# Performance work log

Hardware: AMD Instinct MI355X
Metric: run time of the kernel (lower is better)

## Reference

```python
import jax, jax.numpy as jnp
import numpy as np

DIM = 256; D_STATE = 16; D_CONV = 4; EXPAND = 2; NS = 64
D_INNER = EXPAND * DIM; DT_RANK = (DIM + 15) // 16
B_SZ = 2; H = 64; W = 64


def setup_inputs() -> dict:
    key = jax.random.key(0)
    ks = jax.random.split(key, 32)
    g = lambda i, shape, s=0.02: jax.random.normal(ks[i], shape, dtype=jnp.float32) * s
    inp = {}
    inp["x"] = jax.random.normal(ks[0], (B_SZ, DIM, H, W), dtype=jnp.float32)
    inp["ln_w"] = jnp.ones((DIM,), jnp.float32)
    inp["ln_b"] = jnp.zeros((DIM,), jnp.float32)
    inp["in_proj_w"] = g(1, (2 * D_INNER, DIM))
    for suf, base in (("", 2), ("_b", 10), ("_s", 18)):
        inp["conv_w" + suf] = g(base, (D_INNER, D_CONV), 0.1)
        inp["conv_b" + suf] = g(base + 1, (D_INNER,), 0.1)
        inp["x_proj_w" + suf] = g(base + 2, (DT_RANK + 2 * D_STATE, D_INNER))
        inp["dt_proj_w" + suf] = g(base + 3, (D_INNER, DT_RANK), 0.1)
        inp["dt_proj_b" + suf] = g(base + 4, (D_INNER,), 0.5)
        inp["D" + suf] = jnp.ones((D_INNER,), jnp.float32)
    A_log = jnp.tile(jnp.log(jnp.arange(1, D_STATE + 1, dtype=jnp.float32)), (D_INNER, 1))
    inp["A_log"] = A_log
    inp["A_log_b"] = A_log
    inp["A_log_s"] = A_log
    inp["out_proj_w"] = g(26, (DIM, D_INNER))
    return inp


def _silu(x):
    return x * jax.nn.sigmoid(x)


def _causal_conv(x, w, b):
    # x: (B, L, D); w: (D, K) depthwise causal conv along L
    K = w.shape[1]; L = x.shape[1]
    xp = jnp.pad(x, ((0, 0), (K - 1, 0), (0, 0)))
    y = b
    for k in range(K):
        y = y + xp[:, k:k + L, :] * w[:, k]
    return y


def _ssm_dir(x, z, conv_w, conv_b, x_proj_w, dt_proj_w, dt_proj_b, A_log, Dp):
    # one directional Mamba inner fn (no out_proj); x, z: (B, L, d_inner)
    Bsz, L, Din = x.shape
    xc = _silu(_causal_conv(x, conv_w, conv_b))
    x_dbl = xc @ x_proj_w.T  # (B, L, dt_rank + 2*d_state)
    dt_r = x_dbl[..., :DT_RANK]
    Bm = x_dbl[..., DT_RANK:DT_RANK + D_STATE]
    Cm = x_dbl[..., DT_RANK + D_STATE:]
    dt = jax.nn.softplus(dt_r @ dt_proj_w.T + dt_proj_b)  # (B, L, d_inner)
    A = -jnp.exp(A_log)  # (d_inner, d_state)

    def step(h, inp):
        dt_t, x_t, B_t, C_t = inp
        dA = jnp.exp(dt_t[..., None] * A)  # (B, d_inner, d_state)
        h = dA * h + (dt_t * x_t)[..., None] * B_t[:, None, :]
        return h, jnp.einsum('bds,bs->bd', h, C_t)

    h0 = jnp.zeros((Bsz, Din, D_STATE), x.dtype)
    _, ys = jax.lax.scan(step, h0, (dt.transpose(1, 0, 2), xc.transpose(1, 0, 2),
                                    Bm.transpose(1, 0, 2), Cm.transpose(1, 0, 2)))
    y = ys.transpose(1, 0, 2) + xc * Dp
    return y * _silu(z)


def reference(x, ln_w, ln_b, in_proj_w,
              conv_w, conv_b, x_proj_w, dt_proj_w, dt_proj_b, D,
              conv_w_b, conv_b_b, x_proj_w_b, dt_proj_w_b, dt_proj_b_b, D_b,
              conv_w_s, conv_b_s, x_proj_w_s, dt_proj_w_s, dt_proj_b_s, D_s,
              A_log, A_log_b, A_log_s, out_proj_w):
    Bsz, C, Hh, Ww = x.shape
    L = Hh * Ww
    xf = x.reshape(Bsz, C, L).transpose(0, 2, 1)  # (B, L, C)
    mu = xf.mean(-1, keepdims=True)
    var = ((xf - mu) ** 2).mean(-1, keepdims=True)
    xn = (xf - mu) / jnp.sqrt(var + 1e-5) * ln_w + ln_b
    xz = xn @ in_proj_w.T  # (B, L, 2*d_inner), shared across directions
    xin, z = xz[..., :D_INNER], xz[..., D_INNER:]
    # forward scan
    y_f = _ssm_dir(xin, z, conv_w, conv_b, x_proj_w, dt_proj_w, dt_proj_b, A_log, D)
    # backward scan (flip sequence, scan, flip back)
    y_b = _ssm_dir(xin[:, ::-1], z[:, ::-1], conv_w_b, conv_b_b, x_proj_w_b,
                   dt_proj_w_b, dt_proj_b_b, A_log_b, D_b)[:, ::-1]
    # slice-interleaved scan: 'b (s i) d -> b (i s) d' with s = NS slices
    def il(t):
        return t.reshape(Bsz, NS, L // NS, D_INNER).transpose(0, 2, 1, 3).reshape(Bsz, L, D_INNER)
    def dil(t):
        return t.reshape(Bsz, L // NS, NS, D_INNER).transpose(0, 2, 1, 3).reshape(Bsz, L, D_INNER)
    y_s = dil(_ssm_dir(il(xin), il(z), conv_w_s, conv_b_s, x_proj_w_s,
                       dt_proj_w_s, dt_proj_b_s, A_log_s, D_s))
    out = (y_f + y_b + y_s) @ out_proj_w.T  # (B, L, C)
    return x + out.transpose(0, 2, 1).reshape(Bsz, C, Hh, Ww)
```

## Files before the change

### kernel.cpp

```cpp
#include <hip/hip_runtime.h>
#include <hip/hip_bf16.h>
#include <cstdint>

#define B_SZ 2
#define DIM 256
#define L_SEQ 4096
#define D_INNER 512
#define DT_RANK 16
#define D_STATE 16
#define NCHUNK 128
#define CHUNK 32

static constexpr size_t SZ_BIG_SH = (size_t)B_SZ * L_SEQ * D_INNER;
static constexpr size_t F_DIR  = (size_t)B_SZ * NCHUNK * D_STATE * D_INNER;
static constexpr size_t SD_DIR = (size_t)B_SZ * NCHUNK * D_INNER;

typedef __attribute__((ext_vector_type(8))) short short8v;
typedef __attribute__((ext_vector_type(4))) short short4v;
typedef __attribute__((ext_vector_type(4))) float f32x4;

__device__ __forceinline__ float silu_f(float v) {
    return v / (1.0f + __expf(-v));
}
__device__ __forceinline__ float softplus_fast(float v) {
    return (v > 15.0f) ? v : __logf(1.0f + __expf(v));
}
__device__ __forceinline__ short f2bf(float f) {
    uint32_t u = __float_as_uint(f);
    u += 0x7fffu + ((u >> 16) & 1u);
    return (short)(u >> 16);
}
__device__ __forceinline__ float bf2f(short s) {
    return __uint_as_float(((uint32_t)(uint16_t)s) << 16);
}
__device__ __forceinline__ int dir_map(int p, int dm) {
    if (dm == 0) return p;
    if (dm == 1) return (L_SEQ - 1) - p;
    return ((p & 63) << 6) | (p >> 6);
}
__device__ __forceinline__ void pow_dA(float r1, float* dA) {
    const float r2 = r1 * r1, r4 = r2 * r2, r8 = r4 * r4;
    dA[0] = r1;         dA[1] = r2;         dA[2] = r2 * r1;    dA[3] = r4;
    dA[4] = r4 * r1;    dA[5] = r4 * r2;    dA[6] = r4 * dA[2]; dA[7] = r8;
    dA[8] = r8 * r1;    dA[9] = r8 * r2;    dA[10] = r8 * dA[2]; dA[11] = r8 * r4;
    dA[12] = r8 * dA[4]; dA[13] = r8 * dA[5]; dA[14] = r8 * dA[6]; dA[15] = r8 * r8;
}

__global__ __launch_bounds__(256) void k_cvt(
    const float* __restrict__ Wi, const float* __restrict__ Wo,
    const float* __restrict__ xp0, const float* __restrict__ xp1, const float* __restrict__ xp2,
    const float* __restrict__ dw0, const float* __restrict__ dw1, const float* __restrict__ dw2,
    short* __restrict__ Wib, short* __restrict__ Wob,
    short* __restrict__ xpwb, short* __restrict__ dtwb)
{
    const int idx = blockIdx.x * 256 + threadIdx.x;
    const float* src; short* dst; int off;
    if (idx < 65536)        { src = Wi; dst = Wib; off = idx; }
    else if (idx < 98304)   { src = Wo; dst = Wob; off = idx - 65536; }
    else if (idx < 116736)  {
        int k = idx - 98304; const int d = k / 6144; k -= d * 6144;
        src = d == 0 ? xp0 : (d == 1 ? xp1 : xp2);
        dst = xpwb + (size_t)d * 24576; off = k;
    } else {
        int k = idx - 116736; const int d = k / 2048; k -= d * 2048;
        src = d == 0 ? dw0 : (d == 1 ? dw1 : dw2);
        dst = dtwb + (size_t)d * 8192; off = k;
    }
    const float4 v = *(const float4*)(src + (size_t)off * 4);
    short4v p = {f2bf(v.x), f2bf(v.y), f2bf(v.z), f2bf(v.w)};
    *(short4v*)(dst + (size_t)off * 4) = p;
}

__global__ __launch_bounds__(256) void k_ln_t(
    const float* __restrict__ x, const float* __restrict__ lnw,
    const float* __restrict__ lnb, short* __restrict__ xnb)
{
    __shared__ float xt[64][257];
    __shared__ float red[2][4][64];
    __shared__ float muS[64], rsS[64];
    __shared__ float lnwS[DIM], lnbS[DIM];

    const int b  = blockIdx.x >> 6;
    const int l0 = (blockIdx.x & 63) << 6;
    const int t  = threadIdx.x;
    lnwS[t] = lnw[t]; lnbS[t] = lnb[t];

    const float* xb = x + (size_t)b * DIM * L_SEQ + l0;
#pragma unroll
    for (int it = 0; it < 16; ++it) {
        const int idx = it * 256 + t;
        const int c = idx >> 4, pos = (idx & 15) << 2;
        const float4 v = *(const float4*)(xb + (size_t)c * L_SEQ + pos);
        xt[pos + 0][c] = v.x; xt[pos + 1][c] = v.y;
        xt[pos + 2][c] = v.z; xt[pos + 3][c] = v.w;
    }
    __syncthreads();
    {
        const int l = t & 63, cq = t >> 6;
        float sum = 0.f, sq = 0.f;
        for (int c = cq * 64; c < cq * 64 + 64; ++c) {
            const float v = xt[l][c];
            sum += v; sq += v * v;
        }
        red[0][cq][l] = sum; red[1][cq][l] = sq;
    }
    __syncthreads();
    if (t < 64) {
        const float s  = red[0][0][t] + red[0][1][t] + red[0][2][t] + red[0][3][t];
        const float q2 = red[1][0][t] + red[1][1][t] + red[1][2][t] + red[1][3][t];
        const float mu  = s * (1.0f / DIM);
        const float var = q2 * (1.0f / DIM) - mu * mu;
        muS[t] = mu; rsS[t] = rsqrtf(var + 1e-5f);
    }
    __syncthreads();
#pragma unroll
    for (int it = 0; it < 32; ++it) {
        const int idx = it * 256 + t;
        const int l = idx >> 7, cp = (idx & 127) << 1;
        const float mu = muS[l], rs = rsS[l];
        short2 p;
        p.x = f2bf((xt[l][cp + 0] - mu) * rs * lnwS[cp + 0] + lnbS[cp + 0]);
        p.y = f2bf((xt[l][cp + 1] - mu) * rs * lnwS[cp + 1] + lnbS[cp + 1]);
        *(short2*)(xnb + (size_t)((b * L_SEQ) + l0 + l) * DIM + cp) = p;
    }
}

__global__ __launch_bounds__(256) void k_inproj_mfma(
    const short* __restrict__ xnb, const short* __restrict__ Wib,
    short* __restrict__ xinb, short* __restrict__ szb)
{
    const int mblk = blockIdx.x >> 2;
    const int q    = blockIdx.x & 3;
    const int t = threadIdx.x;
    const int w = t >> 6, l = t & 63;
    const int m0 = mblk * 64 + w * 16;
    const int n0 = q * 256;
    const int lrow = l & 15, lk = l >> 4;

    short8v a[8];
    {
        const short* ap = xnb + (size_t)(m0 + lrow) * DIM + lk * 8;
#pragma unroll
        for (int kk = 0; kk < 8; ++kk)
            a[kk] = *(const short8v*)(ap + kk * 32);
    }

#pragma unroll 4
    for (int nf = 0; nf < 16; ++nf) {
        const int n = n0 + nf * 16 + lrow;
        const short* bp = Wib + (size_t)n * DIM + lk * 8;
        f32x4 acc = {0.f, 0.f, 0.f, 0.f};
#pragma unroll
        for (int kk = 0; kk < 8; ++kk)
            acc = __builtin_amdgcn_mfma_f32_16x16x32_bf16(
                a[kk], *(const short8v*)(bp + kk * 32), acc, 0, 0, 0);
        const int col = n;
        const int r0  = m0 + lk * 4;
        if (n0 < D_INNER) {
#pragma unroll
            for (int j = 0; j < 4; ++j)
                xinb[(size_t)(r0 + j) * D_INNER + col] = f2bf(acc[j]);
        } else {
#pragma unroll
            for (int j = 0; j < 4; ++j)
                szb[(size_t)(r0 + j) * D_INNER + (col - D_INNER)] = f2bf(silu_f(acc[j]));
        }
    }
}

__global__ __launch_bounds__(256) void k_conv3(
    const short* __restrict__ xinb,
    const float* __restrict__ cw0, const float* __restrict__ cw1, const float* __restrict__ cw2,
    const float* __restrict__ cb0, const float* __restrict__ cb1, const float* __restrict__ cb2,
    short* __restrict__ xcbb, int dir_base, size_t xcb_str)
{
    const int rel = blockIdx.x >> 9;
    const int rem = blockIdx.x & 511;
    const int dir = dir_base + rel;
    const int b   = rem >> 8;
    const int p0  = (rem & 255) << 4;
    const int t   = threadIdx.x;

    const float* cw = dir == 0 ? cw0 : (dir == 1 ? cw1 : cw2);
    const float* cb = dir == 0 ? cb0 : (dir == 1 ? cb1 : cb2);
    short* xcb = xcbb + (size_t)rel * xcb_str;

    __shared__ short s[19][D_INNER];
    for (int i = 0; i < 19; ++i) {
        const int pk = p0 - 3 + i;
        short2 v = {0, 0};
        if (pk >= 0) {
            const int lo = dir_map(pk, dir);
            v = *(const short2*)(xinb + ((size_t)b * L_SEQ + lo) * D_INNER + t * 2);
        }
        *(short2*)&s[i][t * 2] = v;
    }
    __syncthreads();

#pragma unroll
    for (int half = 0; half < 2; ++half) {
        const int d = half * 256 + t;
        const float4 wv = *(const float4*)(cw + d * 4);
        const float bb = cb[d];
        float x0 = bf2f(s[0][d]), x1 = bf2f(s[1][d]), x2 = bf2f(s[2][d]);
#pragma unroll
        for (int i = 0; i < 16; ++i) {
            const float x3 = bf2f(s[i + 3][d]);
            const float a = bb + wv.x * x0 + wv.y * x1 + wv.z * x2 + wv.w * x3;
            xcb[((size_t)b * L_SEQ + p0 + i) * D_INNER + d] = f2bf(silu_f(a));
            x0 = x1; x1 = x2; x2 = x3;
        }
    }
}

__global__ __launch_bounds__(256) void k_proj3_mfma(
    const short* __restrict__ xcbb, const short* __restrict__ xpwb,
    const short* __restrict__ dtwb,
    const float* __restrict__ dtb0, const float* __restrict__ dtb1, const float* __restrict__ dtb2,
    short* __restrict__ dtYb, float* __restrict__ bcbuf,
    int dir_base, size_t xcb_str, size_t bc_str)
{
    const int rel = blockIdx.x >> 9;
    const int rem = blockIdx.x & 511;
    const int dir = dir_base + rel;
    const int m0  = rem * 16;
    const int t = threadIdx.x;
    const int w = t >> 6, l = t & 63;
    const int lrow = l & 15, lk = l >> 4;

    const short* xcb = xcbb + (size_t)rel * xcb_str;
    const short* xpw = xpwb + (size_t)dir * (48 * 512);
    const short* dtw = dtwb + (size_t)dir * (512 * 16);
    const float* dtb = dir == 0 ? dtb0 : (dir == 1 ? dtb1 : dtb2);
    short* dt = dtYb + (size_t)dir * SZ_BIG_SH;
    float* bc = bcbuf + (size_t)rel * bc_str;

    __shared__ float red[4][3][16][17];
    __shared__ short xdblb[16][16];
    __shared__ float dtbS[512];

    dtbS[t] = dtb[t]; dtbS[t + 256] = dtb[t + 256];

    short8v a[4];
    {
        const short* ap = xcb + (size_t)(m0 + lrow) * D_INNER + w * 128 + lk * 8;
#pragma unroll
        for (int kk = 0; kk < 4; ++kk)
            a[kk] = *(const short8v*)(ap + kk * 32);
    }

#pragma unroll
    for (int nf = 0; nf < 3; ++nf) {
        f32x4 acc = {0.f, 0.f, 0.f, 0.f};
        const short* bp = xpw + (size_t)(nf * 16 + lrow) * D_INNER + w * 128 + lk * 8;
#pragma unroll
        for (int kk = 0; kk < 4; ++kk)
            acc = __builtin_amdgcn_mfma_f32_16x16x32_bf16(
                a[kk], *(const short8v*)(bp + kk * 32), acc, 0, 0, 0);
#pragma unroll
        for (int j = 0; j < 4; ++j)
            red[w][nf][lk * 4 + j][lrow] = acc[j];
    }
    __syncthreads();

#pragma unroll
    for (int i = 0; i < 3; ++i) {
        const int nf = i;
        const int row = (t >> 4) & 15, col = t & 15;
        const float v = red[0][nf][row][col] + red[1][nf][row][col]
                      + red[2][nf][row][col] + red[3][nf][row][col];
        if (nf == 0) xdblb[row][col] = f2bf(v);
        else         bc[(size_t)(m0 + row) * 32 + (nf - 1) * 16 + col] = v;
    }
    __syncthreads();

    short8v adt = {0, 0, 0, 0, 0, 0, 0, 0};
    if (lk < 2) adt = *(const short8v*)&xdblb[lrow][lk * 8];

#pragma unroll
    for (int nbw = 0; nbw < 8; ++nbw) {
        const int nb = w * 8 + nbw;
        short8v bdt = {0, 0, 0, 0, 0, 0, 0, 0};
        if (lk < 2) bdt = *(const short8v*)(dtw + (size_t)(nb * 16 + lrow) * 16 + lk * 8);
        f32x4 acc = {0.f, 0.f, 0.f, 0.f};
        acc = __builtin_amdgcn_mfma_f32_16x16x32_bf16(adt, bdt, acc, 0, 0, 0);
        const int d = nb * 16 + lrow;
        const float bias = dtbS[d];
#pragma unroll
        for (int j = 0; j < 4; ++j)
            dt[(size_t)(m0 + lk * 4 + j) * D_INNER + d] = f2bf(softplus_fast(acc[j] + bias));
    }
}

__device__ __forceinline__ bool fast_vote(const float* Al_d, int t, int* flagS) {
    bool ok = true;
    const float a0 = __expf(Al_d[0]);
#pragma unroll
    for (int s = 1; s < 16; ++s) {
        const float v = __expf(Al_d[s]);
        const float e = (float)(s + 1) * a0;
        ok = ok && (fabsf(v - e) <= 1e-3f * e);
    }
    if (t == 0) *flagS = 1;
    __syncthreads();
    if (!ok) *flagS = 0;
    __syncthreads();
    return *flagS != 0;
}

template<bool FAST>
__device__ __forceinline__ void scan1_body(
    const short* dtp, const short* xcp, const float* bcp,
    short (*dts)[256], short (*xcs)[256], float (*bcs)[16],
    const float* Al_d, int t, float* F_o, float* SD_o)
{
    float As20, As2[16];
    if (FAST) {
        As20 = -__expf(Al_d[0]) * 1.44269504f;
    } else {
#pragma unroll
        for (int s = 0; s < 16; ++s) As2[s] = -__expf(Al_d[s]) * 1.44269504f;
        As20 = As2[0];
    }
    float h[16];
#pragma unroll
    for (int s = 0; s < 16; ++s) h[s] = 0.f;
    float sumdt = 0.f;

    for (int tile = 0; tile < CHUNK / 16; ++tile) {
        const int p0 = tile * 16;
#pragma unroll
        for (int rep = 0; rep < 2; ++rep) {
            const int idx = rep * 256 + t;
            const int jr = idx >> 5, c8 = (idx & 31) << 3;
            *(short8v*)&dts[jr][c8] = *(const short8v*)(dtp + (size_t)(p0 + jr) * D_INNER + c8);
            *(short8v*)&xcs[jr][c8] = *(const short8v*)(xcp + (size_t)(p0 + jr) * D_INNER + c8);
        }
        if (t < 64) {
            const int jr = t >> 2, c4 = (t & 3) << 2;
            *(float4*)&bcs[jr][c4] = *(const float4*)(bcp + (size_t)(p0 + jr) * 32 + c4);
        }
        __syncthreads();

#pragma unroll
        for (int j = 0; j < 16; ++j) {
            const float dtv = bf2f(dts[j][t]);
            const float xv  = bf2f(xcs[j][t]);
            sumdt += dtv;
            const float dtx = dtv * xv;
            float Bv[16];
#pragma unroll
            for (int s4 = 0; s4 < 4; ++s4) {
                const float4 bb = *(const float4*)&bcs[j][s4 * 4];
                Bv[s4 * 4 + 0] = bb.x; Bv[s4 * 4 + 1] = bb.y;
                Bv[s4 * 4 + 2] = bb.z; Bv[s4 * 4 + 3] = bb.w;
            }
            if (FAST) {
                float dA[16];
                pow_dA(exp2f(dtv * As20), dA);
#pragma unroll
                for (int s = 0; s < 16; ++s)
                    h[s] = fmaf(dA[s], h[s], dtx * Bv[s]);
            } else {
#pragma unroll
                for (int s = 0; s < 16; ++s)
                    h[s] = fmaf(exp2f(dtv * As2[s]), h[s], dtx * Bv[s]);
            }
        }
        __syncthreads();
    }
#pragma unroll
    for (int s = 0; s < 16; ++s)
        F_o[(size_t)s * D_INNER] = h[s];
    *SD_o = sumdt;
}

template<bool FAST>
__device__ __forceinline__ void scan2_body(
    short* dtp, const short* xcp, const float* bcp,
    short (*dts)[256], short (*xcs)[256], float (*bcs)[32],
    const float* Al_d, int t, float Dv, const float* Hin_o)
{
    float As20, As2[16];
    if (FAST) {
        As20 = -__expf(Al_d[0]) * 1.44269504f;
    } else {
#pragma unroll
        for (int s = 0; s < 16; ++s) As2[s] = -__expf(Al_d[s]) * 1.44269504f;
        As20 = As2[0];
    }
    float h[16];
#pragma unroll
    for (int s = 0; s < 16; ++s)
        h[s] = Hin_o[(size_t)s * D_INNER];

    for (int tile = 0; tile < CHUNK / 16; ++tile) {
        const int p0 = tile * 16;
#pragma unroll
        for (int rep = 0; rep < 2; ++rep) {
            const int idx = rep * 256 + t;
            const int jr = idx >> 5, c8 = (idx & 31) << 3;
            *(short8v*)&dts[jr][c8] = *(const short8v*)(dtp + (size_t)(p0 + jr) * D_INNER + c8);
            *(short8v*)&xcs[jr][c8] = *(const short8v*)(xcp + (size_t)(p0 + jr) * D_INNER + c8);
        }
        if (t < 128) {
            const int jr = t >> 3, c4 = (t & 7) << 2;
            *(float4*)&bcs[jr][c4] = *(const float4*)(bcp + (size_t)(p0 + jr) * 32 + c4);
        }
        __syncthreads();

#pragma unroll
        for (int j = 0; j < 16; ++j) {
            const float dtv = bf2f(dts[j][t]);
            const float xv  = bf2f(xcs[j][t]);
            const float dtx = dtv * xv;
            float Bv[16], Cv[16];
#pragma unroll
            for (int s4 = 0; s4 < 4; ++s4) {
                const float4 bb = *(const float4*)&bcs[j][s4 * 4];
                const float4 cc = *(const float4*)&bcs[j][16 + s4 * 4];
                Bv[s4 * 4 + 0] = bb.x; Bv[s4 * 4 + 1] = bb.y;
                Bv[s4 * 4 + 2] = bb.z; Bv[s4 * 4 + 3] = bb.w;
                Cv[s4 * 4 + 0] = cc.x; Cv[s4 * 4 + 1] = cc.y;
                Cv[s4 * 4 + 2] = cc.z; Cv[s4 * 4 + 3] = cc.w;
            }
            float y = xv * Dv;
            if (FAST) {
                float dA[16];
                pow_dA(exp2f(dtv * As20), dA);
#pragma unroll
                for (int s = 0; s < 16; ++s) {
                    h[s] = fmaf(dA[s], h[s], dtx * Bv[s]);
                    y = fmaf(h[s], Cv[s], y);
                }
            } else {
#pragma unroll
                for (int s = 0; s < 16; ++s) {
                    h[s] = fmaf(exp2f(dtv * As2[s]), h[s], dtx * Bv[s]);
                    y = fmaf(h[s], Cv[s], y);
                }
            }
            dtp[(size_t)(p0 + j) * D_INNER + t] = f2bf(y);
        }
        __syncthreads();
    }
}

__global__ __launch_bounds__(256, 4) void k_scan1(
    const short* __restrict__ dtYb, const short* __restrict__ xcbb,
    const float* __restrict__ bcb,
    const float* __restrict__ Al0, const float* __restrict__ Al1, const float* __restrict__ Al2,
    float* __restrict__ Fg, float* __restrict__ SDg,
    int dir_base, size_t xcb_str, size_t bc_str)
{
    const int rel = blockIdx.x >> 9;
    const int rem = blockIdx.x & 511;
    const int dir = dir_base + rel;
    const int b     = rem >> 8;
    const int chunk = (rem >> 1) & 127;
    const int half  = rem & 1;
    const int t = threadIdx.x;
    const int d = half * 256 + t;

    const short* dtg = dtYb + (size_t)dir * SZ_BIG_SH;
    const short* xcg = xcbb + (size_t)rel * xcb_str;
    const float* bcg = bcb + (size_t)rel * bc_str;
    const float* Al = dir == 0 ? Al0 : (dir == 1 ? Al1 : Al2);
    float* F  = Fg  + (size_t)rel * F_DIR;
    float* SD = SDg + (size_t)rel * SD_DIR;

    __shared__ short dts[16][256];
    __shared__ short xcs[16][256];
    __shared__ float bcs[16][16];
    __shared__ int flagS;

    const size_t rowbase = (size_t)b * L_SEQ + chunk * CHUNK;
    const short* dtp = dtg + rowbase * D_INNER + half * 256;
    const short* xcp = xcg + rowbase * D_INNER + half * 256;
    const float* bcp = bcg + rowbase * 32;
    const float* Al_d = Al + d * D_STATE;
    const size_t fo  = ((size_t)b * NCHUNK + chunk) * (D_STATE * D_INNER) + d;
    const size_t sdo = ((size_t)b * NCHUNK + chunk) * D_INNER + d;

    const bool fast = fast_vote(Al_d, t, &flagS);
    if (fast) scan1_body<true >(dtp, xcp, bcp, dts, xcs, bcs, Al_d, t, F + fo, SD + sdo);
    else      scan1_body<false>(dtp, xcp, bcp, dts, xcs, bcs, Al_d, t, F + fo, SD + sdo);
}

__global__ __launch_bounds__(256) void k_comb(
    float* __restrict__ Fg, const float* __restrict__ SDg,
    const float* __restrict__ Al0, const float* __restrict__ Al1, const float* __restrict__ Al2,
    int dir_base)
{
    const int rel = blockIdx.x >> 6;
    const int dir = dir_base + rel;
    const int gid = (blockIdx.x & 63) * 256 + threadIdx.x;
    const int b   = gid >> 13;
    const int rem = gid & 8191;
    const int s   = rem >> 9;
    const int d   = rem & 511;

    const float* Al = dir == 0 ? Al0 : (dir == 1 ? Al1 : Al2);
    const float As2 = -__expf(Al[d * D_STATE + s]) * 1.44269504f;

    float* F        = Fg  + (size_t)rel * F_DIR;
    const float* SD = SDg + (size_t)rel * SD_DIR;

    float h = 0.f;
    for (int c = 0; c < NCHUNK; ++c) {
        const size_t base = (size_t)(b * NCHUNK + c);
        const size_t i  = (base << 13) + rem;
        const float sd  = SD[(base << 9) + d];
        const float P   = exp2f(As2 * sd);
        const float fv  = F[i];
        F[i] = h;
        h = fmaf(P, h, fv);
    }
}

__global__ __launch_bounds__(256, 4) void k_scan2(
    short* dtYb,
    const short* __restrict__ xcbb, const float* __restrict__ bcb,
    const float* __restrict__ Al0, const float* __restrict__ Al1, const float* __restrict__ Al2,
    const float* __restrict__ Dp0, const float* __restrict__ Dp1, const float* __restrict__ Dp2,
    const float* __restrict__ Hing,
    int dir_base, size_t xcb_str, size_t bc_str)
{
    const int rel = blockIdx.x >> 9;
    const int rem = blockIdx.x & 511;
    const int dir = dir_base + rel;
    const int b     = rem >> 8;
    const int chunk = (rem >> 1) & 127;
    const int half  = rem & 1;
    const int t = threadIdx.x;
    const int d = half * 256 + t;

    short* dtg      = dtYb + (size_t)dir * SZ_BIG_SH;
    const short* xcg = xcbb + (size_t)rel * xcb_str;
    const float* bcg = bcb + (size_t)rel * bc_str;
    const float* Al  = dir == 0 ? Al0 : (dir == 1 ? Al1 : Al2);
    const float* Dpp = dir == 0 ? Dp0 : (dir == 1 ? Dp1 : Dp2);
    const float* Hin = Hing + (size_t)rel * F_DIR;

    __shared__ short dts[16][256];
    __shared__ short xcs[16][256];
    __shared__ float bcs[16][32];
    __shared__ int flagS;

    const size_t rowbase = (size_t)b * L_SEQ + chunk * CHUNK;
    short* dtp       = dtg + rowbase * D_INNER + half * 256;
    const short* xcp = xcg + rowbase * D_INNER + half * 256;
    const float* bcp = bcg + rowbase * 32;
    const float* Al_d = Al + d * D_STATE;
    const float Dv = Dpp[d];
    const size_t fo = ((size_t)b * NCHUNK + chunk) * (D_STATE * D_INNER) + d;

    const bool fast = fast_vote(Al_d, t, &flagS);
    if (fast) scan2_body<true >(dtp, xcp, bcp, dts, xcs, bcs, Al_d, t, Dv, Hin + fo);
    else      scan2_body<false>(dtp, xcp, bcp, dts, xcs, bcs, Al_d, t, Dv, Hin + fo);
}

__global__ __launch_bounds__(256) void k_out3_mfma(
    const short* __restrict__ yall, const short* __restrict__ szb,
    const short* __restrict__ Wob, const float* __restrict__ x,
    float* __restrict__ out)
{
    __shared__ short ytb[32][512];
    const int tile = blockIdx.x;
    const int b  = tile >> 7;
    const int l0 = (tile & 127) << 5;
    const int t  = threadIdx.x;

    const short* y0 = yall;
    const short* y1 = yall + SZ_BIG_SH;
    const short* y2 = yall + 2 * SZ_BIG_SH;
    const size_t rb = (size_t)b * L_SEQ;

#pragma unroll
    for (int it = 0; it < 8; ++it) {
        const int idx = it * 256 + t;
        const int r  = idx >> 6;
        const int c8 = idx & 63;
        const int lrow = l0 + r;
        const int p1 = (L_SEQ - 1) - lrow;
        const int p2 = ((lrow & 63) << 6) | (lrow >> 6);
        const short8v s0 = *(const short8v*)(y0 + (rb + lrow) * D_INNER + c8 * 8);
        const short8v s1 = *(const short8v*)(y1 + (rb + p1)   * D_INNER + c8 * 8);
        const short8v s2 = *(const short8v*)(y2 + (rb + p2)   * D_INNER + c8 * 8);
        const short8v sv = *(const short8v*)(szb + (rb + lrow) * D_INNER + c8 * 8);
        short8v pk;
#pragma unroll
        for (int i = 0; i < 8; ++i)
            pk[i] = f2bf((bf2f(s0[i]) + bf2f(s1[i]) + bf2f(s2[i])) * bf2f(sv[i]));
        *(short8v*)&ytb[r][(c8 ^ (r & 7)) * 8] = pk;
    }
    __syncthreads();

    const int w = t >> 6, l = t & 63;
    const int lrow = l & 15, lk = l >> 4;
    const int nf = w & 1;
    const int j0 = (w >> 1) * 128;
    const int brow = nf * 16 + lrow;

    f32x4 acc[8];
#pragma unroll
    for (int jf = 0; jf < 8; ++jf) acc[jf] = {0.f, 0.f, 0.f, 0.f};

#pragma unroll 4
    for (int kk = 0; kk < 16; ++kk) {
        const int c8 = kk * 4 + lk;
        const short8v bfrag = *(const short8v*)&ytb[brow][(c8 ^ (brow & 7)) * 8];
#pragma unroll
        for (int jf = 0; jf < 8; ++jf) {
            const short8v afrag = *(const short8v*)(
                Wob + (size_t)(j0 + jf * 16 + lrow) * D_INNER + kk * 32 + lk * 8);
            acc[jf] = __builtin_amdgcn_mfma_f32_16x16x32_bf16(afrag, bfrag, acc[jf], 0, 0, 0);
        }
    }

    const int lcol = l0 + nf * 16 + lrow;
#pragma unroll
    for (int jf = 0; jf < 8; ++jf) {
        const int jr0 = j0 + jf * 16 + lk * 4;
#pragma unroll
        for (int j = 0; j < 4; ++j) {
            const size_t o = ((size_t)b * DIM + jr0 + j) * L_SEQ + lcol;
            out[o] = x[o] + acc[jf][j];
        }
    }
}

extern "C" void kernel_launch(void* const* d_in, const int* in_sizes, int n_in,
                              void* d_out, int out_size, void* d_ws, size_t ws_size,
                              hipStream_t stream)
{
    const float* x       = (const float*)d_in[0];
    const float* ln_w    = (const float*)d_in[1];
    const float* ln_b    = (const float*)d_in[2];
    const float* in_proj = (const float*)d_in[3];
    const float* conv_w[3] = {(const float*)d_in[4],  (const float*)d_in[10], (const float*)d_in[16]};
    const float* conv_b[3] = {(const float*)d_in[5],  (const float*)d_in[11], (const float*)d_in[17]};
    const float* xpw[3]    = {(const float*)d_in[6],  (const float*)d_in[12], (const float*)d_in[18]};
    const float* dtw[3]    = {(const float*)d_in[7],  (const float*)d_in[13], (const float*)d_in[19]};
    const float* dtb[3]    = {(const float*)d_in[8],  (const float*)d_in[14], (const float*)d_in[20]};
    const float* Dp[3]     = {(const float*)d_in[9],  (const float*)d_in[15], (const float*)d_in[21]};
    const float* A_log[3]  = {(const float*)d_in[22], (const float*)d_in[23], (const float*)d_in[24]};
    const float* out_proj  = (const float*)d_in[25];
    float* out = (float*)d_out;
    (void)in_sizes; (void)n_in; (void)out_size;

    const size_t NROW   = (size_t)B_SZ * L_SEQ;
    const size_t SZ_XNB = NROW * DIM / 2;
    const size_t SZ_WIB = 262144 / 2;
    const size_t SZ_WOB = 131072 / 2;
    const size_t SZ_XPW = 3 * 24576 / 2;
    const size_t SZ_DTW = 3 * 8192 / 2;
    const size_t SZ_BH  = NROW * D_INNER / 2;
    const size_t SZ_BC  = NROW * 32;

    const size_t need_merged =
        SZ_XNB + SZ_WIB + SZ_WOB + SZ_XPW + SZ_DTW +
        2 * SZ_BH + 3 * SZ_BH + 3 * SZ_BH + 3 * SZ_BC + 3 * (F_DIR + SD_DIR);
    const bool merged = ws_size >= need_merged * sizeof(float);
    const int ndir = merged ? 3 : 1;
    const size_t xcb_str = merged ? (SZ_BH * 2) : 0;
    const size_t bc_str  = merged ? SZ_BC : 0;

    float* ws   = (float*)d_ws;
    float* p    = ws;
    short* xnb  = (short*)p;  p += SZ_XNB;
    short* Wib  = (short*)p;  p += SZ_WIB;
    short* Wob  = (short*)p;  p += SZ_WOB;
    short* xpwb = (short*)p;  p += SZ_XPW;
    short* dtwb = (short*)p;  p += SZ_DTW;
    short* xinb = (short*)p;  p += SZ_BH;
    short* szb  = (short*)p;  p += SZ_BH;
    short* dtYb = (short*)p;  p += 3 * SZ_BH;
    short* xcbb = (short*)p;  p += (size_t)ndir * SZ_BH;
    float* bc   = p;          p += (size_t)ndir * SZ_BC;
    float* Fg   = p;          p += (size_t)ndir * F_DIR;
    float* SDg  = p;          p += (size_t)ndir * SD_DIR;

    k_cvt<<<dim3(480), dim3(256), 0, stream>>>(
        in_proj, out_proj, xpw[0], xpw[1], xpw[2], dtw[0], dtw[1], dtw[2],
        Wib, Wob, xpwb, dtwb);
    k_ln_t<<<dim3(B_SZ * 64), dim3(256), 0, stream>>>(x, ln_w, ln_b, xnb);
    k_inproj_mfma<<<dim3(512), dim3(256), 0, stream>>>(xnb, Wib, xinb, szb);

    for (int d0 = 0; d0 < 3; d0 += ndir) {
        k_conv3<<<dim3(512 * ndir), dim3(256), 0, stream>>>(
            xinb, conv_w[0], conv_w[1], conv_w[2],
            conv_b[0], conv_b[1], conv_b[2], xcbb, d0, xcb_str);
        k_proj3_mfma<<<dim3(512 * ndir), dim3(256), 0, stream>>>(
            xcbb, xpwb, dtwb, dtb[0], dtb[1], dtb[2],
            dtYb, bc, d0, xcb_str, bc_str);
        k_scan1<<<dim3(512 * ndir), dim3(256), 0, stream>>>(
            dtYb, xcbb, bc, A_log[0], A_log[1], A_log[2], Fg, SDg,
            d0, xcb_str, bc_str);
        k_comb<<<dim3(64 * ndir), dim3(256), 0, stream>>>(
            Fg, SDg, A_log[0], A_log[1], A_log[2], d0);
        k_scan2<<<dim3(512 * ndir), dim3(256), 0, stream>>>(
            dtYb, xcbb, bc, A_log[0], A_log[1], A_log[2],
            Dp[0], Dp[1], Dp[2], Fg, d0, xcb_str, bc_str);
    }

    k_out3_mfma<<<dim3(256), dim3(256), 0, stream>>>(
        dtYb, szb, Wob, x, out);
}
```

Baseline: 235.8 us.

## Recompute dt projection inside scan kernels and store chunk states in bf16

The projection kernel now writes only the 16-wide low-rank dt input instead of the full 512-wide softplus dt tensor. Both scan passes rebuild dt per channel with a 16-term dot product plus softplus, and the scan output goes to a separate y buffer. Chunk carry states F are also stored in bf16 rather than fp32. This removes large dt write/read traffic and halves F traffic, at the cost of extra ALU work in the scans being done twice and reduced precision of the carried states.

```diff
diff --git a/kernel.cpp b/kernel.cpp
--- a/kernel.cpp
+++ b/kernel.cpp
@@ -14,6 +14,7 @@
 static constexpr size_t SZ_BIG_SH = (size_t)B_SZ * L_SEQ * D_INNER;
 static constexpr size_t F_DIR  = (size_t)B_SZ * NCHUNK * D_STATE * D_INNER;
 static constexpr size_t SD_DIR = (size_t)B_SZ * NCHUNK * D_INNER;
+static constexpr size_t DTR_DIR = (size_t)B_SZ * L_SEQ * DT_RANK;
 
 typedef __attribute__((ext_vector_type(8))) short short8v;
 typedef __attribute__((ext_vector_type(4))) short short4v;
@@ -215,9 +216,7 @@
 
 __global__ __launch_bounds__(256) void k_proj3_mfma(
     const short* __restrict__ xcbb, const short* __restrict__ xpwb,
-    const short* __restrict__ dtwb,
-    const float* __restrict__ dtb0, const float* __restrict__ dtb1, const float* __restrict__ dtb2,
-    short* __restrict__ dtYb, float* __restrict__ bcbuf,
+    short* __restrict__ dtrb, float* __restrict__ bcbuf,
     int dir_base, size_t xcb_str, size_t bc_str)
 {
     const int rel = blockIdx.x >> 9;
@@ -230,16 +229,10 @@
 
     const short* xcb = xcbb + (size_t)rel * xcb_str;
     const short* xpw = xpwb + (size_t)dir * (48 * 512);
-    const short* dtw = dtwb + (size_t)dir * (512 * 16);
-    const float* dtb = dir == 0 ? dtb0 : (dir == 1 ? dtb1 : dtb2);
-    short* dt = dtYb + (size_t)dir * SZ_BIG_SH;
+    short* dtr = dtrb + (size_t)dir * DTR_DIR;
     float* bc = bcbuf + (size_t)rel * bc_str;
 
     __shared__ float red[4][3][16][17];
-    __shared__ short xdblb[16][16];
-    __shared__ float dtbS[512];
-
-    dtbS[t] = dtb[t]; dtbS[t + 256] = dtb[t + 256];
 
     short8v a[4];
     {
@@ -269,26 +262,8 @@
         const int row = (t >> 4) & 15, col = t & 15;
         const float v = red[0][nf][row][col] + red[1][nf][row][col]
                       + red[2][nf][row][col] + red[3][nf][row][col];
-        if (nf == 0) xdblb[row][col] = f2bf(v);
+        if (nf == 0) dtr[(size_t)(m0 + row) * DT_RANK + col] = f2bf(v);
         else         bc[(size_t)(m0 + row) * 32 + (nf - 1) * 16 + col] = v;
-    }
-    __syncthreads();
-
-    short8v adt = {0, 0, 0, 0, 0, 0, 0, 0};
-    if (lk < 2) adt = *(const short8v*)&xdblb[lrow][lk * 8];
-
-#pragma unroll
-    for (int nbw = 0; nbw < 8; ++nbw) {
-        const int nb = w * 8 + nbw;
-        short8v bdt = {0, 0, 0, 0, 0, 0, 0, 0};
-        if (lk < 2) bdt = *(const short8v*)(dtw + (size_t)(nb * 16 + lrow) * 16 + lk * 8);
-        f32x4 acc = {0.f, 0.f, 0.f, 0.f};
-        acc = __builtin_amdgcn_mfma_f32_16x16x32_bf16(adt, bdt, acc, 0, 0, 0);
-        const int d = nb * 16 + lrow;
-        const float bias = dtbS[d];
-#pragma unroll
-        for (int j = 0; j < 4; ++j)
-            dt[(size_t)(m0 + lk * 4 + j) * D_INNER + d] = f2bf(softplus_fast(acc[j] + bias));
     }
 }
 
@@ -310,10 +285,16 @@
 
 template<bool FAST>
 __device__ __forceinline__ void scan1_body(
-    const short* dtp, const short* xcp, const float* bcp,
-    short (*dts)[256], short (*xcs)[256], float (*bcs)[16],
-    const float* Al_d, int t, float* F_o, float* SD_o)
-{
+    const short* dtrp,
+    const short* xcp, const float* bcp,
+    short (*dtrS)[16], short (*xcs)[256], float (*bcs)[16],
+    const float* Al_d, const short* dtw_d, float bias,
+    int t, short* F_o, float* SD_o)
+{
+    float wdt[16];
+#pragma unroll
+    for (int k = 0; k < 16; ++k) wdt[k] = bf2f(dtw_d[k]);
+
     float As20, As2[16];
     if (FAST) {
         As20 = -__expf(Al_d[0]) * 1.44269504f;
@@ -329,11 +310,11 @@
 
     for (int tile = 0; tile < CHUNK / 16; ++tile) {
         const int p0 = tile * 16;
+        dtrS[t >> 4][t & 15] = dtrp[(size_t)(p0 + (t >> 4)) * DT_RANK + (t & 15)];
 #pragma unroll
         for (int rep = 0; rep < 2; ++rep) {
             const int idx = rep * 256 + t;
             const int jr = idx >> 5, c8 = (idx & 31) << 3;
-            *(short8v*)&dts[jr][c8] = *(const short8v*)(dtp + (size_t)(p0 + jr) * D_INNER + c8);
             *(short8v*)&xcs[jr][c8] = *(const short8v*)(xcp + (size_t)(p0 + jr) * D_INNER + c8);
         }
         if (t < 64) {
@@ -344,7 +325,11 @@
 
 #pragma unroll
         for (int j = 0; j < 16; ++j) {
-            const float dtv = bf2f(dts[j][t]);
+            float a = bias;
+#pragma unroll
+            for (int k = 0; k < 16; ++k)
+                a = fmaf(bf2f(dtrS[j][k]), wdt[k], a);
+            const float dtv = softplus_fast(a);
             const float xv  = bf2f(xcs[j][t]);
             sumdt += dtv;
             const float dtx = dtv * xv;
@@ -371,16 +356,22 @@
     }
 #pragma unroll
     for (int s = 0; s < 16; ++s)
-        F_o[(size_t)s * D_INNER] = h[s];
+        F_o[(size_t)s * D_INNER] = f2bf(h[s]);
     *SD_o = sumdt;
 }
 
 template<bool FAST>
 __device__ __forceinline__ void scan2_body(
-    short* dtp, const short* xcp, const float* bcp,
-    short (*dts)[256], short (*xcs)[256], float (*bcs)[32],
-    const float* Al_d, int t, float Dv, const float* Hin_o)
-{
+    const short* dtrp, const short* xcp, const float* bcp,
+    short* yp,
+    short (*dtrS)[16], short (*xcs)[256], float (*bcs)[32],
+    const float* Al_d, const short* dtw_d, float bias,
+    int t, float Dv, const short* Hin_o)
+{
+    float wdt[16];
+#pragma unroll
+    for (int k = 0; k < 16; ++k) wdt[k] = bf2f(dtw_d[k]);
+
     float As20, As2[16];
     if (FAST) {
         As20 = -__expf(Al_d[0]) * 1.44269504f;
@@ -392,15 +383,15 @@
     float h[16];
 #pragma unroll
     for (int s = 0; s < 16; ++s)
-        h[s] = Hin_o[(size_t)s * D_INNER];
+        h[s] = bf2f(Hin_o[(size_t)s * D_INNER]);
 
     for (int tile = 0; tile < CHUNK / 16; ++tile) {
         const int p0 = tile * 16;
+        dtrS[t >> 4][t & 15] = dtrp[(size_t)(p0 + (t >> 4)) * DT_RANK + (t & 15)];
 #pragma unroll
         for (int rep = 0; rep < 2; ++rep) {
             const int idx = rep * 256 + t;
             const int jr = idx >> 5, c8 = (idx & 31) << 3;
-            *(short8v*)&dts[jr][c8] = *(const short8v*)(dtp + (size_t)(p0 + jr) * D_INNER + c8);
             *(short8v*)&xcs[jr][c8] = *(const short8v*)(xcp + (size_t)(p0 + jr) * D_INNER + c8);
         }
         if (t < 128) {
@@ -411,7 +402,11 @@
 
 #pragma unroll
         for (int j = 0; j < 16; ++j) {
-            const float dtv = bf2f(dts[j][t]);
+            float a = bias;
+#pragma unroll
+            for (int k = 0; k < 16; ++k)
+                a = fmaf(bf2f(dtrS[j][k]), wdt[k], a);
+            const float dtv = softplus_fast(a);
             const float xv  = bf2f(xcs[j][t]);
             const float dtx = dtv * xv;
             float Bv[16], Cv[16];
@@ -440,17 +435,18 @@
                     y = fmaf(h[s], Cv[s], y);
                 }
             }
-            dtp[(size_t)(p0 + j) * D_INNER + t] = f2bf(y);
+            yp[(size_t)(p0 + j) * D_INNER + t] = f2bf(y);
         }
         __syncthreads();
     }
 }
 
 __global__ __launch_bounds__(256, 4) void k_scan1(
-    const short* __restrict__ dtYb, const short* __restrict__ xcbb,
-    const float* __restrict__ bcb,
+    const short* __restrict__ dtrb, const short* __restrict__ xcbb,
+    const float* __restrict__ bcb, const short* __restrict__ dtwb,
+    const float* __restrict__ dtb0, const float* __restrict__ dtb1, const float* __restrict__ dtb2,
     const float* __restrict__ Al0, const float* __restrict__ Al1, const float* __restrict__ Al2,
-    float* __restrict__ Fg, float* __restrict__ SDg,
+    short* __restrict__ Fg, float* __restrict__ SDg,
     int dir_base, size_t xcb_str, size_t bc_str)
 {
     const int rel = blockIdx.x >> 9;
@@ -462,33 +458,37 @@
     const int t = threadIdx.x;
     const int d = half * 256 + t;
 
-    const short* dtg = dtYb + (size_t)dir * SZ_BIG_SH;
-    const short* xcg = xcbb + (size_t)rel * xcb_str;
-    const float* bcg = bcb + (size_t)rel * bc_str;
-    const float* Al = dir == 0 ? Al0 : (dir == 1 ? Al1 : Al2);
-    float* F  = Fg  + (size_t)rel * F_DIR;
+    const short* dtrg = dtrb + (size_t)dir * DTR_DIR;
+    const short* xcg  = xcbb + (size_t)rel * xcb_str;
+    const float* bcg  = bcb + (size_t)rel * bc_str;
+    const short* dtw  = dtwb + (size_t)dir * (512 * 16);
+    const float* dtb  = dir == 0 ? dtb0 : (dir == 1 ? dtb1 : dtb2);
+    const float* Al   = dir == 0 ? Al0 : (dir == 1 ? Al1 : Al2);
+    short* F  = Fg  + (size_t)rel * F_DIR;
     float* SD = SDg + (size_t)rel * SD_DIR;
 
-    __shared__ short dts[16][256];
+    __shared__ short dtrS[16][16];
     __shared__ short xcs[16][256];
     __shared__ float bcs[16][16];
     __shared__ int flagS;
 
     const size_t rowbase = (size_t)b * L_SEQ + chunk * CHUNK;
-    const short* dtp = dtg + rowbase * D_INNER + half * 256;
-    const short* xcp = xcg + rowbase * D_INNER + half * 256;
-    const float* bcp = bcg + rowbase * 32;
+    const short* dtrp = dtrg + rowbase * DT_RANK;
+    const short* xcp  = xcg + rowbase * D_INNER + half * 256;
+    const float* bcp  = bcg + rowbase * 32;
     const float* Al_d = Al + d * D_STATE;
     const size_t fo  = ((size_t)b * NCHUNK + chunk) * (D_STATE * D_INNER) + d;
     const size_t sdo = ((size_t)b * NCHUNK + chunk) * D_INNER + d;
 
     const bool fast = fast_vote(Al_d, t, &flagS);
-    if (fast) scan1_body<true >(dtp, xcp, bcp, dts, xcs, bcs, Al_d, t, F + fo, SD + sdo);
-    else      scan1_body<false>(dtp, xcp, bcp, dts, xcs, bcs, Al_d, t, F + fo, SD + sdo);
+    if (fast) scan1_body<true >(dtrp, xcp, bcp, dtrS, xcs, bcs, Al_d,
+                                dtw + d * 16, dtb[d], t, F + fo, SD + sdo);
+    else      scan1_body<false>(dtrp, xcp, bcp, dtrS, xcs, bcs, Al_d,
+                                dtw + d * 16, dtb[d], t, F + fo, SD + sdo);
 }
 
 __global__ __launch_bounds__(256) void k_comb(
-    float* __restrict__ Fg, const float* __restrict__ SDg,
+    short* __restrict__ Fg, const float* __restrict__ SDg,
     const float* __restrict__ Al0, const float* __restrict__ Al1, const float* __restrict__ Al2,
     int dir_base)
 {
@@ -503,7 +503,7 @@
     const float* Al = dir == 0 ? Al0 : (dir == 1 ? Al1 : Al2);
     const float As2 = -__expf(Al[d * D_STATE + s]) * 1.44269504f;
 
-    float* F        = Fg  + (size_t)rel * F_DIR;
+    short* F        = Fg  + (size_t)rel * F_DIR;
     const float* SD = SDg + (size_t)rel * SD_DIR;
 
     float h = 0.f;
@@ -512,18 +512,19 @@
         const size_t i  = (base << 13) + rem;
         const float sd  = SD[(base << 9) + d];
         const float P   = exp2f(As2 * sd);
-        const float fv  = F[i];
-        F[i] = h;
+        const float fv  = bf2f(F[i]);
+        F[i] = f2bf(h);
         h = fmaf(P, h, fv);
     }
 }
 
 __global__ __launch_bounds__(256, 4) void k_scan2(
-    short* dtYb,
-    const short* __restrict__ xcbb, const float* __restrict__ bcb,
+    const short* __restrict__ dtrb, const short* __restrict__ xcbb,
+    const float* __restrict__ bcb, const short* __restrict__ dtwb,
+    const float* __restrict__ dtb0, const float* __restrict__ dtb1, const float* __restrict__ dtb2,
     const float* __restrict__ Al0, const float* __restrict__ Al1, const float* __restrict__ Al2,
     const float* __restrict__ Dp0, const float* __restrict__ Dp1, const float* __restrict__ Dp2,
-    const float* __restrict__ Hing,
+    const short* __restrict__ Hing, short* __restrict__ ybg,
     int dir_base, size_t xcb_str, size_t bc_str)
 {
     const int rel = blockIdx.x >> 9;
@@ -535,29 +536,35 @@
     const int t = threadIdx.x;
     const int d = half * 256 + t;
 
-    short* dtg      = dtYb + (size_t)dir * SZ_BIG_SH;
-    const short* xcg = xcbb + (size_t)rel * xcb_str;
-    const float* bcg = bcb + (size_t)rel * bc_str;
-    const float* Al  = dir == 0 ? Al0 : (dir == 1 ? Al1 : Al2);
-    const float* Dpp = dir == 0 ? Dp0 : (dir == 1 ? Dp1 : Dp2);
-    const float* Hin = Hing + (size_t)rel * F_DIR;
-
-    __shared__ short dts[16][256];
+    const short* dtrg = dtrb + (size_t)dir * DTR_DIR;
+    const short* xcg  = xcbb + (size_t)rel * xcb_str;
+    const float* bcg  = bcb + (size_t)rel * bc_str;
+    const short* dtw  = dtwb + (size_t)dir * (512 * 16);
+    const float* dtb  = dir == 0 ? dtb0 : (dir == 1 ? dtb1 : dtb2);
+    const float* Al   = dir == 0 ? Al0 : (dir == 1 ? Al1 : Al2);
+    const float* Dpp  = dir == 0 ? Dp0 : (dir == 1 ? Dp1 : Dp2);
+    const short* Hin  = Hing + (size_t)rel * F_DIR;
+    short* yg         = ybg + (size_t)dir * SZ_BIG_SH;
+
+    __shared__ short dtrS[16][16];
     __shared__ short xcs[16][256];
     __shared__ float bcs[16][32];
     __shared__ int flagS;
 
     const size_t rowbase = (size_t)b * L_SEQ + chunk * CHUNK;
-    short* dtp       = dtg + rowbase * D_INNER + half * 256;
-    const short* xcp = xcg + rowbase * D_INNER + half * 256;
-    const float* bcp = bcg + rowbase * 32;
+    const short* dtrp = dtrg + rowbase * DT_RANK;
+    const short* xcp  = xcg + rowbase * D_INNER + half * 256;
+    short* yp         = yg + rowbase * D_INNER + half * 256;
+    const float* bcp  = bcg + rowbase * 32;
     const float* Al_d = Al + d * D_STATE;
     const float Dv = Dpp[d];
     const size_t fo = ((size_t)b * NCHUNK + chunk) * (D_STATE * D_INNER) + d;
 
     const bool fast = fast_vote(Al_d, t, &flagS);
-    if (fast) scan2_body<true >(dtp, xcp, bcp, dts, xcs, bcs, Al_d, t, Dv, Hin + fo);
-    else      scan2_body<false>(dtp, xcp, bcp, dts, xcs, bcs, Al_d, t, Dv, Hin + fo);
+    if (fast) scan2_body<true >(dtrp, xcp, bcp, yp, dtrS, xcs, bcs, Al_d,
+                                dtw + d * 16, dtb[d], t, Dv, Hin + fo);
+    else      scan2_body<false>(dtrp, xcp, bcp, yp, dtrS, xcs, bcs, Al_d,
+                                dtw + d * 16, dtb[d], t, Dv, Hin + fo);
 }
 
 __global__ __launch_bounds__(256) void k_out3_mfma(
@@ -657,10 +664,13 @@
     const size_t SZ_DTW = 3 * 8192 / 2;
     const size_t SZ_BH  = NROW * D_INNER / 2;
     const size_t SZ_BC  = NROW * 32;
+    const size_t SZ_F   = F_DIR / 2;
+    const size_t SZ_DTR = DTR_DIR / 2;
 
     const size_t need_merged =
         SZ_XNB + SZ_WIB + SZ_WOB + SZ_XPW + SZ_DTW +
-        2 * SZ_BH + 3 * SZ_BH + 3 * SZ_BH + 3 * SZ_BC + 3 * (F_DIR + SD_DIR);
+        2 * SZ_BH + 3 * SZ_BH + 3 * SZ_DTR + 3 * SZ_BH + 3 * SZ_BC +
+        3 * (SZ_F + SD_DIR);
     const bool merged = ws_size >= need_merged * sizeof(float);
     const int ndir = merged ? 3 : 1;
     const size_t xcb_str = merged ? (SZ_BH * 2) : 0;
@@ -675,10 +685,11 @@
     short* dtwb = (short*)p;  p += SZ_DTW;
     short* xinb = (short*)p;  p += SZ_BH;
     short* szb  = (short*)p;  p += SZ_BH;
-    short* dtYb = (short*)p;  p += 3 * SZ_BH;
+    short* yb   = (short*)p;  p += 3 * SZ_BH;
+    short* dtrb = (short*)p;  p += 3 * SZ_DTR;
     short* xcbb = (short*)p;  p += (size_t)ndir * SZ_BH;
     float* bc   = p;          p += (size_t)ndir * SZ_BC;
-    float* Fg   = p;          p += (size_t)ndir * F_DIR;
+    short* Fg   = (short*)p;  p += (size_t)ndir * SZ_F;
     float* SDg  = p;          p += (size_t)ndir * SD_DIR;
 
     k_cvt<<<dim3(480), dim3(256), 0, stream>>>(
@@ -692,18 +703,19 @@
             xinb, conv_w[0], conv_w[1], conv_w[2],
             conv_b[0], conv_b[1], conv_b[2], xcbb, d0, xcb_str);
         k_proj3_mfma<<<dim3(512 * ndir), dim3(256), 0, stream>>>(
-            xcbb, xpwb, dtwb, dtb[0], dtb[1], dtb[2],
-            dtYb, bc, d0, xcb_str, bc_str);
+            xcbb, xpwb, dtrb, bc, d0, xcb_str, bc_str);
         k_scan1<<<dim3(512 * ndir), dim3(256), 0, stream>>>(
-            dtYb, xcbb, bc, A_log[0], A_log[1], A_log[2], Fg, SDg,
+            dtrb, xcbb, bc, dtwb, dtb[0], dtb[1], dtb[2],
+            A_log[0], A_log[1], A_log[2], Fg, SDg,
             d0, xcb_str, bc_str);
         k_comb<<<dim3(64 * ndir), dim3(256), 0, stream>>>(
             Fg, SDg, A_log[0], A_log[1], A_log[2], d0);
         k_scan2<<<dim3(512 * ndir), dim3(256), 0, stream>>>(
-            dtYb, xcbb, bc, A_log[0], A_log[1], A_log[2],
-            Dp[0], Dp[1], Dp[2], Fg, d0, xcb_str, bc_str);
+            dtrb, xcbb, bc, dtwb, dtb[0], dtb[1], dtb[2],
+            A_log[0], A_log[1], A_log[2],
+            Dp[0], Dp[1], Dp[2], Fg, yb, d0, xcb_str, bc_str);
     }
 
     k_out3_mfma<<<dim3(256), dim3(256), 0, stream>>>(
-        dtYb, szb, Wob, x, out);
-}
+        yb, szb, Wob, x, out);
+}
```

Result: slower. 271.7 us (+15.2%).
